# Optimization experiments

Hardware: AMD Instinct MI355X
Metric: run time of the kernel (lower is better)

The kernel has to match this reference:

```python
import jax, jax.numpy as jnp
import numpy as np

B, S, T, M, D, H = 32, 256, 400, 80, 512, 8


def setup_inputs() -> dict:
    ks = iter(jax.random.split(jax.random.key(0), 64))
    rn = lambda shape, s=0.05: jax.random.normal(next(ks), shape, jnp.float32) * s
    z = lambda shape: jnp.zeros(shape, jnp.float32)
    o = lambda shape: jnp.ones(shape, jnp.float32)
    inp = {
        'encoder_outputs': jax.random.normal(next(ks), (B, S, D), jnp.float32),
        'mel_targets': jax.random.normal(next(ks), (B, T, M), jnp.float32),
        'W_in': rn((M, D)), 'b_in': z(D),
        'Wq': rn((D, D)), 'bq': z(D),
        'Wk': rn((D, D)), 'bk': z(D),
        'Wv': rn((D, D)), 'bv': z(D),
        'Wo': rn((D, D)), 'bo': z(D),
        'W_ih0': rn((4 * D, D + M)), 'W_hh0': rn((4 * D, D)), 'b_ih0': z(4 * D), 'b_hh0': z(4 * D),
        'W_ih1': rn((4 * D, D)), 'W_hh1': rn((4 * D, D)), 'b_ih1': z(4 * D), 'b_hh1': z(4 * D),
        'W_mel': rn((D, M)), 'b_mel': z(M),
        'W_stop': rn((D, 1)), 'b_stop': z(1),
        'pw0': rn((512, M, 5)), 'pb0': z(512),
        'pw1': rn((512, 512, 5)), 'pb1': z(512),
        'pw2': rn((512, 512, 5)), 'pb2': z(512),
        'pw3': rn((512, 512, 5)), 'pb3': z(512),
        'pw4': rn((M, 512, 5)), 'pb4': z(M),
        'g0': o(512), 'be0': z(512), 'g1': o(512), 'be1': z(512),
        'g2': o(512), 'be2': z(512), 'g3': o(512), 'be3': z(512),
    }
    return inp


def _lstm_layer(x, W_ih, W_hh, b_ih, b_hh):
    # x: [B,T,I]. Precompute input contribution for all steps (big matmul), scan only recurrence.
    xg = jnp.einsum('bti,gi->btg', x, W_ih) + b_ih + b_hh  # [B,T,4D]
    Dh = W_hh.shape[1]

    def step(carry, xg_t):
        h, c = carry
        gates = xg_t + h @ W_hh.T
        i, f, g, o_ = jnp.split(gates, 4, axis=-1)  # pytorch gate order i,f,g,o
        c = jax.nn.sigmoid(f) * c + jax.nn.sigmoid(i) * jnp.tanh(g)
        h = jax.nn.sigmoid(o_) * jnp.tanh(c)
        return (h, c), h

    h0 = jnp.zeros((x.shape[0], Dh), x.dtype)
    _, hs = jax.lax.scan(step, (h0, h0), jnp.swapaxes(xg, 0, 1))
    return jnp.swapaxes(hs, 0, 1)  # [B,T,D]


def _conv1d(x, w, b):
    # x: [B,C,T], w: [O,I,K]
    y = jax.lax.conv_general_dilated(x, w, (1,), 'SAME', dimension_numbers=('NCH', 'OIH', 'NCH'))
    return y + b[None, :, None]


def _bn(x, g, be, eps=1e-5):
    # training-mode BatchNorm1d over (N, L) per channel
    mu = jnp.mean(x, axis=(0, 2), keepdims=True)
    var = jnp.mean((x - mu) ** 2, axis=(0, 2), keepdims=True)
    return (x - mu) * jax.lax.rsqrt(var + eps) * g[None, :, None] + be[None, :, None]


def _forward(encoder_outputs, mel_targets, W_in, b_in, Wq, bq, Wk, bk, Wv, bv, Wo, bo,
             W_ih0, W_hh0, b_ih0, b_hh0, W_ih1, W_hh1, b_ih1, b_hh1,
             W_mel, b_mel, W_stop, b_stop,
             pw0, pb0, pw1, pb1, pw2, pb2, pw3, pb3, pw4, pb4,
             g0, be0, g1, be1, g2, be2, g3, be3):
    Bs, Ts, Ms = mel_targets.shape
    Ss = encoder_outputs.shape[1]
    Ds = W_in.shape[1]
    Dh = Ds // H
    # teacher forcing: decoder input at step t is mel_targets[t-1], zeros at t=0
    dec_in = jnp.concatenate([jnp.zeros((Bs, 1, Ms), mel_targets.dtype), mel_targets[:, :-1]], axis=1)
    q_in = dec_in @ W_in + b_in  # [B,T,D]
    qh = (q_in @ Wq + bq).reshape(Bs, Ts, H, Dh)
    kh = (encoder_outputs @ Wk + bk).reshape(Bs, Ss, H, Dh)
    vh = (encoder_outputs @ Wv + bv).reshape(Bs, Ss, H, Dh)
    scores = jnp.einsum('bthd,bshd->bhts', qh, kh) / jnp.sqrt(jnp.float32(Dh))
    attn = jax.nn.softmax(scores, axis=-1)
    ctx = jnp.einsum('bhts,bshd->bthd', attn, vh).reshape(Bs, Ts, Ds)
    attn_out = ctx @ Wo + bo  # [B,T,D]
    lstm_in = jnp.concatenate([attn_out, dec_in], axis=-1)  # [B,T,D+M]
    h1 = _lstm_layer(lstm_in, W_ih0, W_hh0, b_ih0, b_hh0)
    h2 = _lstm_layer(h1, W_ih1, W_hh1, b_ih1, b_hh1)
    mel_outputs = h2 @ W_mel + b_mel   # [B,T,M]
    stop_outputs = h2 @ W_stop + b_stop  # [B,T,1]
    # postnet (dropout omitted; BN in training mode uses batch stats)
    x = jnp.swapaxes(mel_outputs, 1, 2)  # [B,M,T]
    x = jnp.tanh(_bn(_conv1d(x, pw0, pb0), g0, be0))
    x = jnp.tanh(_bn(_conv1d(x, pw1, pb1), g1, be1))
    x = jnp.tanh(_bn(_conv1d(x, pw2, pb2), g2, be2))
    x = jnp.tanh(_bn(_conv1d(x, pw3, pb3), g3, be3))
    x = _conv1d(x, pw4, pb4)
    mel_postnet = mel_outputs + jnp.swapaxes(x, 1, 2)
    return mel_outputs, mel_postnet, stop_outputs


def reference(encoder_outputs, mel_targets, W_in, b_in, Wq, bq, Wk, bk, Wv, bv, Wo, bo,
              W_ih0, W_hh0, b_ih0, b_hh0, W_ih1, W_hh1, b_ih1, b_hh1,
              W_mel, b_mel, W_stop, b_stop,
              pw0, pb0, pw1, pb1, pw2, pb2, pw3, pb3, pw4, pb4,
              g0, be0, g1, be1, g2, be2, g3, be3):
    return _forward(encoder_outputs, mel_targets, W_in, b_in, Wq, bq, Wk, bk, Wv, bv, Wo, bo,
                    W_ih0, W_hh0, b_ih0, b_hh0, W_ih1, W_hh1, b_ih1, b_hh1,
                    W_mel, b_mel, W_stop, b_stop,
                    pw0, pb0, pw1, pb1, pw2, pb2, pw3, pb3, pw4, pb4,
                    g0, be0, g1, be1, g2, be2, g3, be3)
```

## Files before the change

kernel.cpp:

```cpp
#include <hip/hip_runtime.h>
#include <math.h>

#define B_  32
#define S_  256
#define T_  400
#define M_  80
#define D_  512
#define H_  8
#define DH  64
#define BT  (B_*T_)
#define BS  (B_*S_)
#define G4  (4*D_)
#define DM  (D_+M_)
#define NB_ 96

typedef short s16x8 __attribute__((ext_vector_type(8)));
typedef float f32x4 __attribute__((ext_vector_type(4)));
typedef unsigned long long u64;

__device__ __forceinline__ unsigned short f2bf(float f) {
    union { float f; unsigned u; } v; v.f = f;
    unsigned r = v.u + 0x7fffu + ((v.u >> 16) & 1u);
    return (unsigned short)(r >> 16);
}
__device__ __forceinline__ float us2f(unsigned short u) {
    union { unsigned i; float f; } v; v.i = ((unsigned)u) << 16; return v.f;
}
__device__ __forceinline__ uint4 pack8(const float* f) {
    uint4 u;
    u.x = (unsigned)f2bf(f[0]) | ((unsigned)f2bf(f[1]) << 16);
    u.y = (unsigned)f2bf(f[2]) | ((unsigned)f2bf(f[3]) << 16);
    u.z = (unsigned)f2bf(f[4]) | ((unsigned)f2bf(f[5]) << 16);
    u.w = (unsigned)f2bf(f[6]) | ((unsigned)f2bf(f[7]) << 16);
    return u;
}
__device__ __forceinline__ u64 aload(const u64* p) {
    return __hip_atomic_load(p, __ATOMIC_RELAXED, __HIP_MEMORY_SCOPE_AGENT);
}
__device__ __forceinline__ void astore(u64* p, u64 v) {
    __hip_atomic_store(p, v, __ATOMIC_RELAXED, __HIP_MEMORY_SCOPE_AGENT);
}

__global__ __launch_bounds__(256) void k_prep(
    const float* __restrict__ bih1, const float* __restrict__ bhh1,
    float* __restrict__ bsum1,
    int* __restrict__ flags, int* __restrict__ hx2i,
    float* __restrict__ ssum, float* __restrict__ ssq)
{
    int i = blockIdx.x * 256 + threadIdx.x;
    if (i < G4) bsum1[i] = bih1[i] + bhh1[i];
    if (i < 512) { ssum[i] = 0.f; ssq[i] = 0.f; }
    if (i < NB_ * 32) flags[i] = 0;
    if (i < 2 * 32 * 512 / 2) hx2i[i] = 0;
}

__global__ __launch_bounds__(256) void k_w_c4(
    const float* s0, unsigned short* d0p, int n0,
    const float* s1, unsigned short* d1p, int n1,
    const float* s2, unsigned short* d2p, int n2,
    const float* s3, unsigned short* d3p, int n3)
{
    const float* s; unsigned short* d; int n;
    switch (blockIdx.y) {
        case 0: s = s0; d = d0p; n = n0; break;
        case 1: s = s1; d = d1p; n = n1; break;
        case 2: s = s2; d = d2p; n = n2; break;
        default: s = s3; d = d3p; n = n3; break;
    }
    int i = blockIdx.x * 256 + threadIdx.x;
    if (i < n) d[i] = f2bf(s[i]);
}
__global__ __launch_bounds__(256) void k_w_perm0(
    const float* __restrict__ W, unsigned short* __restrict__ dst,
    const float* __restrict__ bih, const float* __restrict__ bhh,
    float* __restrict__ bsum0p)
{
    int i = blockIdx.x * 256 + threadIdx.x;
    if (i < G4 * DM) {
        int np = i / DM, k = i - np * DM;
        int bd = np >> 6, r = np & 63, g = r >> 4, dl = r & 15;
        int ns = g * 512 + bd * 16 + dl;
        dst[i] = f2bf(W[(size_t)ns * DM + k]);
    }
    if (i < G4) {
        int bd = i >> 6, r = i & 63, g = r >> 4, dl = r & 15;
        int ns = g * 512 + bd * 16 + dl;
        bsum0p[i] = bih[ns] + bhh[ns];
    }
}
__global__ __launch_bounds__(256) void k_w_t4(
    const float* s0, unsigned short* d0p, int K0, int N0,
    const float* s1, unsigned short* d1p, int K1, int N1,
    const float* s2, unsigned short* d2p, int K2, int N2,
    const float* s3, unsigned short* d3p, int K3, int N3)
{
    const float* s; unsigned short* d; int K, N;
    switch (blockIdx.y) {
        case 0: s = s0; d = d0p; K = K0; N = N0; break;
        case 1: s = s1; d = d1p; K = K1; N = N1; break;
        case 2: s = s2; d = d2p; K = K2; N = N2; break;
        default: s = s3; d = d3p; K = K3; N = N3; break;
    }
    int i = blockIdx.x * 256 + threadIdx.x;
    if (i < K * N) {
        int n = i / K, k = i - n * K;
        d[i] = f2bf(s[(size_t)k * N + n]);
    }
}
__global__ __launch_bounds__(256) void k_w_conv5(
    const float* s0, unsigned short* d0p, int O0, int C0,
    const float* s1, unsigned short* d1p, int O1, int C1,
    const float* s2, unsigned short* d2p, int O2, int C2,
    const float* s3, unsigned short* d3p, int O3, int C3,
    const float* s4, unsigned short* d4p, int O4, int C4)
{
    const float* s; unsigned short* d; int O, C;
    switch (blockIdx.y) {
        case 0: s = s0; d = d0p; O = O0; C = C0; break;
        case 1: s = s1; d = d1p; O = O1; C = C1; break;
        case 2: s = s2; d = d2p; O = O2; C = C2; break;
        case 3: s = s3; d = d3p; O = O3; C = C3; break;
        default: s = s4; d = d4p; O = O4; C = C4; break;
    }
    int i = blockIdx.x * 256 + threadIdx.x;
    int n = O * C * 5;
    if (i < n) {
        int o = i / (5 * C), rem = i - o * 5 * C;
        int k = rem / C, c = rem - k * C;
        d[i] = f2bf(s[(size_t)o * C * 5 + c * 5 + k]);
    }
}

__global__ __launch_bounds__(256) void k_weff(
    const float* __restrict__ W_in, const float* __restrict__ Wq,
    const float* __restrict__ b_in, const float* __restrict__ bq,
    float* __restrict__ Weff, float* __restrict__ beff)
{
    int idx = blockIdx.x * 256 + threadIdx.x;
    if (idx < M_ * D_) {
        int m = idx / D_, d = idx - m * D_;
        float acc = 0.f;
        for (int j = 0; j < D_; ++j)
            acc += W_in[(size_t)m * D_ + j] * Wq[(size_t)j * D_ + d];
        Weff[idx] = acc;
    }
    if (idx < D_) {
        float acc = bq[idx];
        for (int j = 0; j < D_; ++j)
            acc += b_in[j] * Wq[(size_t)j * D_ + idx];
        beff[idx] = acc;
    }
}

__global__ __launch_bounds__(256) void k_mfma(
    const void* __restrict__ Aptr, int lda, const float* __restrict__ mel, int srcC,
    const unsigned short* __restrict__ Bt,
    void* __restrict__ Cptr, int ldc, const float* __restrict__ bias,
    int M, int N, int K, int mode, int abf16, int cbf16)
{
    __shared__ unsigned short As[128][40];
    __shared__ unsigned short Bs[128][40];
    int tid = threadIdx.x;
    int m0 = blockIdx.x * 128, n0 = blockIdx.y * 128;
    int wave = tid >> 6, lane = tid & 63;
    int wm = (wave >> 1) * 64, wn = (wave & 1) * 64;
    int l15 = lane & 15, quad = lane >> 4;

    f32x4 acc[4][4] = {};

    int srow = tid >> 1, half = tid & 1;
    int arow = m0 + srow;
    bool mok = arow < M;
    int arc = mok ? arow : 0;

    const float* Af = (const float*)Aptr;
    const unsigned short* Ab = (const unsigned short*)Aptr;
    const float* Arow_f = nullptr; const unsigned short* Arow_b = nullptr;
    const float* Mrow = nullptr;
    int bA = 0, tA = 0;
    if (mode == 2) { bA = arc / T_; tA = arc - bA * T_; }
    else {
        if (abf16) Arow_b = Ab + (size_t)arc * lda;
        else       Arow_f = Af + (size_t)arc * lda;
        if (mode == 1) {
            int tt = arc % T_;
            if (tt > 0) Mrow = mel + (size_t)(arc - 1) * M_;
        }
    }
    int brow = n0 + srow;
    bool nok = brow < N;
    const unsigned short* Brow = Bt + (size_t)(nok ? brow : 0) * K;
    const uint4 z4 = make_uint4(0, 0, 0, 0);

    for (int k0 = 0; k0 < K; k0 += 32) {
        int ks = k0 + half * 16;
        uint4 a0, a1;
        if (!mok || ks >= K) { a0 = z4; a1 = z4; }
        else if (mode == 2) {
            int sg = ks / srcC;
            int cc = ks - sg * srcC;
            int tt = tA + sg - 2;
            if (tt >= 0 && tt < T_) {
                float tf[16];
                const float4* s = (const float4*)(Af + (size_t)(bA * T_ + tt) * srcC + cc);
                #pragma unroll
                for (int i = 0; i < 4; ++i) {
                    float4 v = s[i];
                    tf[i*4+0] = v.x; tf[i*4+1] = v.y; tf[i*4+2] = v.z; tf[i*4+3] = v.w;
                }
                a0 = pack8(tf); a1 = pack8(tf + 8);
            } else { a0 = z4; a1 = z4; }
        } else if (abf16) {
            const uint4* s = (const uint4*)(Arow_b + ks);
            a0 = s[0]; a1 = s[1];
        } else if (mode == 1 && ks >= D_) {
            if (Mrow) {
                float tf[16];
                const float4* s = (const float4*)(Mrow + (ks - D_));
                #pragma unroll
                for (int i = 0; i < 4; ++i) {
                    float4 v = s[i];
                    tf[i*4+0] = v.x; tf[i*4+1] = v.y; tf[i*4+2] = v.z; tf[i*4+3] = v.w;
                }
                a0 = pack8(tf); a1 = pack8(tf + 8);
            } else { a0 = z4; a1 = z4; }
        } else {
            float tf[16];
            const float4* s = (const float4*)(Arow_f + ks);
            #pragma unroll
            for (int i = 0; i < 4; ++i) {
                float4 v = s[i];
                tf[i*4+0] = v.x; tf[i*4+1] = v.y; tf[i*4+2] = v.z; tf[i*4+3] = v.w;
            }
            a0 = pack8(tf); a1 = pack8(tf + 8);
        }
        *(uint4*)&As[srow][half * 16]     = a0;
        *(uint4*)&As[srow][half * 16 + 8] = a1;

        uint4 b0, b1;
        if (!nok || ks >= K) { b0 = z4; b1 = z4; }
        else {
            const uint4* s = (const uint4*)(Brow + ks);
            b0 = s[0]; b1 = s[1];
        }
        *(uint4*)&Bs[srow][half * 16]     = b0;
        *(uint4*)&Bs[srow][half * 16 + 8] = b1;
        __syncthreads();

        s16x8 af[4], bfr[4];
        #pragma unroll
        for (int i = 0; i < 4; ++i)
            af[i] = *(const s16x8*)&As[wm + i * 16 + l15][quad * 8];
        #pragma unroll
        for (int j = 0; j < 4; ++j)
            bfr[j] = *(const s16x8*)&Bs[wn + j * 16 + l15][quad * 8];
        #pragma unroll
        for (int i = 0; i < 4; ++i)
            #pragma unroll
            for (int j = 0; j < 4; ++j)
                acc[i][j] = __builtin_amdgcn_mfma_f32_16x16x32_bf16(af[i], bfr[j], acc[i][j], 0, 0, 0);
        __syncthreads();
    }

    #pragma unroll
    for (int i = 0; i < 4; ++i) {
        #pragma unroll
        for (int j = 0; j < 4; ++j) {
            int col = n0 + wn + j * 16 + l15;
            if (col >= N) continue;
            float bv = bias ? bias[col] : 0.f;
            #pragma unroll
            for (int r = 0; r < 4; ++r) {
                int row = m0 + wm + i * 16 + quad * 4 + r;
                if (row >= M) continue;
                float v = acc[i][j][r] + bv;
                if (cbf16) ((unsigned short*)Cptr)[(size_t)row * ldc + col] = f2bf(v);
                else       ((float*)Cptr)[(size_t)row * ldc + col] = v;
            }
        }
    }
}

__global__ __launch_bounds__(256) void k_attn(
    const float* __restrict__ mel,
    const float* __restrict__ Weff, const float* __restrict__ beff,
    const float* __restrict__ Kb, const float* __restrict__ Vb,
    float* __restrict__ ctx)
{
    __shared__ float mrow[4][80];
    __shared__ float qs[4][64];
    __shared__ float ps[4][256];
    int w = threadIdx.x >> 6, lane = threadIdx.x & 63;
    int row = blockIdx.x * 4 + w;
    int t = row % T_; int bh = row / T_;
    int h = bh % H_;  int b = bh / H_;

    {
        float v = 0.f;
        if (t > 0) v = mel[(size_t)(b * T_ + (t - 1)) * M_ + lane];
        mrow[w][lane] = v;
        if (lane < 16) {
            float v2 = 0.f;
            if (t > 0) v2 = mel[(size_t)(b * T_ + (t - 1)) * M_ + 64 + lane];
            mrow[w][64 + lane] = v2;
        }
    }
    __syncthreads();
    {
        int d = h * DH + lane;
        float q = beff[d];
        #pragma unroll 8
        for (int m = 0; m < M_; ++m) q += mrow[w][m] * Weff[(size_t)m * D_ + d];
        qs[w][lane] = q;
    }
    __syncthreads();

    const float* Kbase = Kb + (size_t)(b * S_) * D_ + h * DH;
    float sc[4];
    #pragma unroll
    for (int i = 0; i < 4; ++i) {
        int s = lane + i * 64;
        const float4* kr = (const float4*)(Kbase + (size_t)s * D_);
        float acc = 0.f;
        #pragma unroll
        for (int c4 = 0; c4 < 16; ++c4) {
            float4 kv = kr[c4];
            acc += qs[w][c4 * 4 + 0] * kv.x + qs[w][c4 * 4 + 1] * kv.y
                 + qs[w][c4 * 4 + 2] * kv.z + qs[w][c4 * 4 + 3] * kv.w;
        }
        sc[i] = acc * 0.125f;
    }
    float mx = fmaxf(fmaxf(sc[0], sc[1]), fmaxf(sc[2], sc[3]));
    #pragma unroll
    for (int off = 32; off; off >>= 1) mx = fmaxf(mx, __shfl_xor(mx, off, 64));
    float sum = 0.f;
    #pragma unroll
    for (int i = 0; i < 4; ++i) { sc[i] = __expf(sc[i] - mx); sum += sc[i]; }
    #pragma unroll
    for (int off = 32; off; off >>= 1) sum += __shfl_xor(sum, off, 64);
    float inv = 1.f / sum;
    #pragma unroll
    for (int i = 0; i < 4; ++i) ps[w][lane + i * 64] = sc[i] * inv;
    __syncthreads();

    const float* Vbase = Vb + (size_t)(b * S_) * D_ + h * DH + lane;
    float acc = 0.f;
    for (int s = 0; s < S_; ++s) acc += ps[w][s] * Vbase[(size_t)s * D_];
    ctx[(size_t)(b * T_ + t) * D_ + h * DH + lane] = acc;
}

__global__ __launch_bounds__(256) void k_lstm2(
    const unsigned short* __restrict__ xg0,
    const unsigned short* __restrict__ Whh0,
    const unsigned short* __restrict__ Wih1,
    const unsigned short* __restrict__ Whh1,
    const float* __restrict__ bsum1,
    unsigned short* __restrict__ hx1,
    unsigned short* __restrict__ hx2,
    unsigned short* __restrict__ h2seq,
    int* __restrict__ flags)
{
    __shared__ char smem[137856];
    int tid = threadIdx.x;
    int bid = blockIdx.x;
    int lane = tid & 63, wv = tid >> 6;
    int l15 = lane & 15, quad = lane >> 4;

    if (bid < 32) {
        unsigned short* Ws   = (unsigned short*)smem;
        unsigned short* hs   = Ws + 64 * 520;
        float*          gl   = (float*)(smem + 99840);
        unsigned short* hout = (unsigned short*)(smem + 108288);
        int d0 = bid * 16;
        {
            int r = tid >> 2, seg = tid & 3;
            int g = r >> 4, d = r & 15;
            const uint4* src = (const uint4*)(Whh0 + ((size_t)(g * 512 + d0 + d) * 512) + seg * 128);
            uint4* dst = (uint4*)(Ws + r * 520 + seg * 128);
            #pragma unroll
            for (int j = 0; j < 16; ++j) dst[j] = src[j];
        }
        int b_u = tid >> 3, dp = tid & 7;
        float c0r = 0.f, c1r = 0.f;
        __syncthreads();

        for (int i = 0; i <= 400; ++i) {
            if (i < 400) {
                int t = i;
                unsigned xv[4];
                {
                    const unsigned short* xr = xg0 + ((size_t)(b_u * T_ + t) * G4) + bid * 64;
                    #pragma unroll
                    for (int g = 0; g < 4; ++g) xv[g] = *(const unsigned*)(xr + g * 16 + 2 * dp);
                }
                if (t > 0) {
                    const u64* hrd = (const u64*)(hx1 + ((t + 1) & 1) * (32 * 512));
                    #pragma unroll
                    for (int it = 0; it < 8; ++it) {
                        int u = it * 256 + tid;
                        int row = u >> 6, c8 = u & 63;
                        u64 lo = aload(hrd + 2 * u);
                        u64 hi = aload(hrd + 2 * u + 1);
                        u64* d = (u64*)(hs + row * 520 + c8 * 8);
                        d[0] = lo; d[1] = hi;
                    }
                    __syncthreads();
                    f32x4 acc0 = {}, acc1 = {};
                    #pragma unroll
                    for (int k0 = 0; k0 < 512; k0 += 32) {
                        s16x8 af = *(const s16x8*)(Ws + (wv * 16 + l15) * 520 + k0 + quad * 8);
                        s16x8 b0 = *(const s16x8*)(hs + l15 * 520 + k0 + quad * 8);
                        s16x8 b1 = *(const s16x8*)(hs + (16 + l15) * 520 + k0 + quad * 8);
                        acc0 = __builtin_amdgcn_mfma_f32_16x16x32_bf16(af, b0, acc0, 0, 0, 0);
                        acc1 = __builtin_amdgcn_mfma_f32_16x16x32_bf16(af, b1, acc1, 0, 0, 0);
                    }
                    #pragma unroll
                    for (int r = 0; r < 4; ++r) {
                        gl[(wv * 16 + quad * 4 + r) * 33 + l15]      = acc0[r];
                        gl[(wv * 16 + quad * 4 + r) * 33 + 16 + l15] = acc1[r];
                    }
                }
                __syncthreads();
                {
                    float h2v[2];
                    #pragma unroll
                    for (int q = 0; q < 2; ++q) {
                        int d = 2 * dp + q;
                        float iv = us2f((unsigned short)(xv[0] >> (16 * q)));
                        float fv = us2f((unsigned short)(xv[1] >> (16 * q)));
                        float gv = us2f((unsigned short)(xv[2] >> (16 * q)));
                        float ov = us2f((unsigned short)(xv[3] >> (16 * q)));
                        if (t > 0) {
                            iv += gl[(0 * 16 + d) * 33 + b_u];
                            fv += gl[(1 * 16 + d) * 33 + b_u];
                            gv += gl[(2 * 16 + d) * 33 + b_u];
                            ov += gl[(3 * 16 + d) * 33 + b_u];
                        }
                        float si = 1.f / (1.f + __expf(-iv));
                        float sf = 1.f / (1.f + __expf(-fv));
                        float so = 1.f / (1.f + __expf(-ov));
                        float tg = tanhf(gv);
                        float cold = (t > 0) ? (q ? c1r : c0r) : 0.f;
                        float c = sf * cold + si * tg;
                        float h = so * tanhf(c);
                        if (q) c1r = c; else c0r = c;
                        h2v[q] = h;
                    }
                    unsigned pk = (unsigned)f2bf(h2v[0]) | ((unsigned)f2bf(h2v[1]) << 16);
                    *(unsigned*)(hout + b_u * 16 + 2 * dp) = pk;
                }
                __syncthreads();
                if (tid < 64) {
                    int b = tid >> 1, hf = tid & 1;
                    uint4 v = *(const uint4*)(hout + b * 16 + hf * 8);
                    u64 lo = ((u64)v.y << 32) | v.x;
                    u64 hi = ((u64)v.w << 32) | v.z;
                    u64* dst = (u64*)(hx1 + (t & 1) * (32 * 512) + (size_t)b * 512 + d0 + hf * 8);
                    astore(dst, lo); astore(dst + 1, hi);
                }
            }
            if (i < 400) {
                __syncthreads();
                if (tid == 0)
                    __hip_atomic_store(flags + bid * 32, i + 1, __ATOMIC_RELAXED, __HIP_MEMORY_SCOPE_AGENT);
                if (tid < NB_) {
                    while (__hip_atomic_load(flags + tid * 32, __ATOMIC_RELAXED, __HIP_MEMORY_SCOPE_AGENT) < i + 1)
                        __builtin_amdgcn_s_sleep(1);
                }
                __syncthreads();
            }
        }
    } else {
        unsigned short* Wc    = (unsigned short*)smem;
        unsigned short* hcat  = Wc + 32 * 1040;
        float*          gl1   = (float*)(smem + 133120);
        unsigned short* hout1 = (unsigned short*)(smem + 137344);
        int bd1 = bid - 32;
        int d0 = bd1 * 8;
        {
            int r = tid >> 3, seg = tid & 7;
            int g = r >> 3, d = r & 7;
            const unsigned short* wsrc = ((seg < 4) ? Wih1 : Whh1)
                + (size_t)(g * 512 + d0 + d) * 512 + (seg & 3) * 128;
            uint4* wdst = (uint4*)(Wc + r * 1040 + seg * 128);
            const uint4* ws4 = (const uint4*)wsrc;
            #pragma unroll
            for (int j = 0; j < 16; ++j) wdst[j] = ws4[j];
        }
        int dd = tid >> 5, b_u = tid & 31;
        float bs[4];
        #pragma unroll
        for (int g = 0; g < 4; ++g) bs[g] = bsum1[g * 512 + d0 + dd];
        int mt = wv >> 1, nt = wv & 1;
        float creg = 0.f;
        __syncthreads();

        for (int i = 0; i <= 400; ++i) {
            if (i >= 1) {
                int t = i - 1;
                const u64* s1 = (const u64*)(hx1 + ((i - 1) & 1) * (32 * 512));
                const u64* s2 = (const u64*)(hx2 + ((i - 2) & 1) * (32 * 512));
                #pragma unroll
                for (int it = 0; it < 8; ++it) {
                    int u = it * 256 + tid;
                    int row = u >> 6, c8 = u & 63;
                    u64 lo = aload(s1 + 2 * u), hi = aload(s1 + 2 * u + 1);
                    u64* d = (u64*)(hcat + row * 1040 + c8 * 8);
                    d[0] = lo; d[1] = hi;
                    lo = aload(s2 + 2 * u); hi = aload(s2 + 2 * u + 1);
                    d = (u64*)(hcat + row * 1040 + 512 + c8 * 8);
                    d[0] = lo; d[1] = hi;
                }
                __syncthreads();
                f32x4 acc = {};
                #pragma unroll 4
                for (int k0 = 0; k0 < 1024; k0 += 32) {
                    s16x8 af = *(const s16x8*)(Wc + (mt * 16 + l15) * 1040 + k0 + quad * 8);
                    s16x8 bf = *(const s16x8*)(hcat + (nt * 16 + l15) * 1040 + k0 + quad * 8);
                    acc = __builtin_amdgcn_mfma_f32_16x16x32_bf16(af, bf, acc, 0, 0, 0);
                }
                #pragma unroll
                for (int r = 0; r < 4; ++r)
                    gl1[(mt * 16 + quad * 4 + r) * 33 + nt * 16 + l15] = acc[r];
                __syncthreads();
                {
                    float iv = gl1[(0 * 8 + dd) * 33 + b_u] + bs[0];
                    float fv = gl1[(1 * 8 + dd) * 33 + b_u] + bs[1];
                    float gv = gl1[(2 * 8 + dd) * 33 + b_u] + bs[2];
                    float ov = gl1[(3 * 8 + dd) * 33 + b_u] + bs[3];
                    float si = 1.f / (1.f + __expf(-iv));
                    float sf = 1.f / (1.f + __expf(-fv));
                    float so = 1.f / (1.f + __expf(-ov));
                    float tg = tanhf(gv);
                    float cold = (t > 0) ? creg : 0.f;
                    float c = sf * cold + si * tg;
                    float h = so * tanhf(c);
                    creg = c;
                    hout1[b_u * 8 + dd] = f2bf(h);
                }
                __syncthreads();
                if (tid < 32) {
                    uint4 v = *(const uint4*)(hout1 + tid * 8);
                    u64 lo = ((u64)v.y << 32) | v.x;
                    u64 hi = ((u64)v.w << 32) | v.z;
                    u64* dst = (u64*)(hx2 + (t & 1) * (32 * 512) + (size_t)tid * 512 + d0);
                    astore(dst, lo); astore(dst + 1, hi);
                    *(uint4*)(h2seq + ((size_t)tid * T_ + t) * 512 + d0) = v;
                }
            }
            if (i < 400) {
                __syncthreads();
                if (tid == 0)
                    __hip_atomic_store(flags + bid * 32, i + 1, __ATOMIC_RELAXED, __HIP_MEMORY_SCOPE_AGENT);
                if (tid < NB_) {
                    while (__hip_atomic_load(flags + tid * 32, __ATOMIC_RELAXED, __HIP_MEMORY_SCOPE_AGENT) < i + 1)
                        __builtin_amdgcn_s_sleep(1);
                }
                __syncthreads();
            }
        }
    }
}

__global__ __launch_bounds__(256) void k_stop(
    const unsigned short* __restrict__ h2, const float* __restrict__ W,
    const float* __restrict__ bsc, float* __restrict__ out)
{
    int w = threadIdx.x >> 6, lane = threadIdx.x & 63;
    int row = blockIdx.x * 4 + w;
    const unsigned short* hr = h2 + (size_t)row * 512 + lane * 8;
    float acc = 0.f;
    #pragma unroll
    for (int j = 0; j < 8; ++j) acc += us2f(hr[j]) * W[lane * 8 + j];
    #pragma unroll
    for (int off = 32; off; off >>= 1) acc += __shfl_xor(acc, off, 64);
    if (lane == 0) out[row] = acc + bsc[0];
}

__global__ __launch_bounds__(256) void k_stats_part(
    const float* __restrict__ x, float* __restrict__ ssum, float* __restrict__ ssq)
{
    int r0 = blockIdx.x * 50;
    int c1 = threadIdx.x, c2 = threadIdx.x + 256;
    float s1 = 0.f, q1 = 0.f, s2 = 0.f, q2 = 0.f;
    for (int r = r0; r < r0 + 50; ++r) {
        float v1 = x[(size_t)r * 512 + c1]; s1 += v1; q1 += v1 * v1;
        float v2 = x[(size_t)r * 512 + c2]; s2 += v2; q2 += v2 * v2;
    }
    atomicAdd(&ssum[c1], s1); atomicAdd(&ssq[c1], q1);
    atomicAdd(&ssum[c2], s2); atomicAdd(&ssq[c2], q2);
}
__global__ __launch_bounds__(256) void k_stats_fin(
    float* __restrict__ ssum, float* __restrict__ ssq,
    const float* __restrict__ gw, const float* __restrict__ bw,
    float* __restrict__ scale, float* __restrict__ shift)
{
    int c = blockIdx.x * 256 + threadIdx.x;
    if (c < 512) {
        float mean = ssum[c] / (float)BT;
        float var  = ssq[c] / (float)BT - mean * mean;
        float scv  = gw[c] * rsqrtf(var + 1e-5f);
        scale[c] = scv;
        shift[c] = bw[c] - mean * scv;
        ssum[c] = 0.f; ssq[c] = 0.f;
    }
}

__global__ __launch_bounds__(256) void k_bnact(
    float* __restrict__ x, int C,
    const float* __restrict__ scale, const float* __restrict__ shift)
{
    int idx = blockIdx.x * 256 + threadIdx.x;
    if (idx < BT * C) {
        int c = idx % C;
        x[idx] = tanhf(scale[c] * x[idx] + shift[c]);
    }
}

__global__ __launch_bounds__(256) void k_residual(
    const float* __restrict__ mel, float* __restrict__ out)
{
    int i = blockIdx.x * 256 + threadIdx.x;
    if (i < BT * M_) out[i] += mel[i];
}

extern "C" void kernel_launch(void* const* d_in, const int* in_sizes, int n_in,
                              void* d_out, int out_size, void* d_ws, size_t ws_size,
                              hipStream_t stream)
{
    const float* enc    = (const float*)d_in[0];
    const float* mel_t  = (const float*)d_in[1];
    const float* W_in   = (const float*)d_in[2];
    const float* b_in   = (const float*)d_in[3];
    const float* Wq     = (const float*)d_in[4];  const float* bq = (const float*)d_in[5];
    const float* Wk     = (const float*)d_in[6];  const float* bk = (const float*)d_in[7];
    const float* Wv     = (const float*)d_in[8];  const float* bv = (const float*)d_in[9];
    const float* Wo     = (const float*)d_in[10]; const float* bo = (const float*)d_in[11];
    const float* W_ih0  = (const float*)d_in[12]; const float* W_hh0 = (const float*)d_in[13];
    const float* b_ih0  = (const float*)d_in[14]; const float* b_hh0 = (const float*)d_in[15];
    const float* W_ih1  = (const float*)d_in[16]; const float* W_hh1 = (const float*)d_in[17];
    const float* b_ih1  = (const float*)d_in[18]; const float* b_hh1 = (const float*)d_in[19];
    const float* W_mel  = (const float*)d_in[20]; const float* b_mel = (const float*)d_in[21];
    const float* W_stop = (const float*)d_in[22]; const float* b_stop = (const float*)d_in[23];
    const float* pw0 = (const float*)d_in[24]; const float* pb0 = (const float*)d_in[25];
    const float* pw1 = (const float*)d_in[26]; const float* pb1 = (const float*)d_in[27];
    const float* pw2 = (const float*)d_in[28]; const float* pb2 = (const float*)d_in[29];
    const float* pw3 = (const float*)d_in[30]; const float* pb3 = (const float*)d_in[31];
    const float* pw4 = (const float*)d_in[32]; const float* pb4 = (const float*)d_in[33];
    const float* g0 = (const float*)d_in[34]; const float* be0 = (const float*)d_in[35];
    const float* g1 = (const float*)d_in[36]; const float* be1 = (const float*)d_in[37];
    const float* g2 = (const float*)d_in[38]; const float* be2 = (const float*)d_in[39];
    const float* g3 = (const float*)d_in[40]; const float* be3 = (const float*)d_in[41];

    char* p = (char*)d_ws;
    float* Kb  = (float*)(p + 0);
    float* Vb  = (float*)(p + 16777216);
    float* ctx = (float*)(p + 33554432);
    float* ao  = (float*)(p + 0);
    unsigned short* xg0   = (unsigned short*)(p + 26214400);
    unsigned short* h2seq = (unsigned short*)(p + 0);
    float* p_a = (float*)(p + 13107200);
    float* p_b = (float*)(p + 39321600);
    size_t off = 78643200;
    float* bsum0 = (float*)(p + off); off += 8192;
    float* bsum1 = (float*)(p + off); off += 8192;
    unsigned short* hx1 = (unsigned short*)(p + off); off += 65536;
    unsigned short* hx2 = (unsigned short*)(p + off); off += 65536;
    int* flags = (int*)(p + off); off += 12288;
    float* beff = (float*)(p + off); off += 2048;
    float* Weff = (float*)(p + off); off += 163840;
    float* sc0 = (float*)(p + off); off += 2048;
    float* sh0 = (float*)(p + off); off += 2048;
    float* sc1 = (float*)(p + off); off += 2048;
    float* sh1 = (float*)(p + off); off += 2048;
    float* sc2 = (float*)(p + off); off += 2048;
    float* sh2 = (float*)(p + off); off += 2048;
    float* sc3 = (float*)(p + off); off += 2048;
    float* sh3 = (float*)(p + off); off += 2048;
    float* ssum = (float*)(p + off); off += 2048;
    float* ssq  = (float*)(p + off); off += 2048;
    unsigned short* Wk_t   = (unsigned short*)(p + off); off += 524288;
    unsigned short* Wv_t   = (unsigned short*)(p + off); off += 524288;
    unsigned short* Wo_t   = (unsigned short*)(p + off); off += 524288;
    unsigned short* Wmel_t = (unsigned short*)(p + off); off += 81920;
    unsigned short* Wih0_b = (unsigned short*)(p + off); off += 2424832;
    unsigned short* Wih1_b = (unsigned short*)(p + off); off += 2097152;
    unsigned short* Whh0_b = (unsigned short*)(p + off); off += 2097152;
    unsigned short* Whh1_b = (unsigned short*)(p + off); off += 2097152;
    unsigned short* pw0_b  = (unsigned short*)(p + off); off += 409600;
    unsigned short* pw1_b  = (unsigned short*)(p + off); off += 2621440;
    unsigned short* pw2_b  = (unsigned short*)(p + off); off += 2621440;
    unsigned short* pw3_b  = (unsigned short*)(p + off); off += 2621440;
    unsigned short* pw4_b  = (unsigned short*)(p + off); off += 409600;

    float* out_mel  = (float*)d_out;
    float* out_post = out_mel + (size_t)BT * M_;
    float* out_stop = out_post + (size_t)BT * M_;

    dim3 blk(256);
    auto MF = [&](const void* A, int lda, const float* mel, int srcC,
                  const unsigned short* Bt, void* C, int ldc, const float* bias,
                  int M, int N, int K, int mode, int abf16, int cbf16) {
        dim3 g((M + 127) / 128, (N + 127) / 128);
        k_mfma<<<g, blk, 0, stream>>>(A, lda, mel, srcC, Bt, C, ldc, bias, M, N, K, mode, abf16, cbf16);
    };

    k_prep<<<128, blk, 0, stream>>>(b_ih1, b_hh1, bsum1, flags, (int*)hx2, ssum, ssq);
    k_weff<<<160, blk, 0, stream>>>(W_in, Wq, b_in, bq, Weff, beff);
    k_w_perm0<<<4736, blk, 0, stream>>>(W_ih0, Wih0_b, b_ih0, b_hh0, bsum0);
    {
        dim3 gc(4096, 4);
        k_w_c4<<<gc, blk, 0, stream>>>(W_ih1, Wih1_b, G4 * D_,
                                       W_hh0, Whh0_b, G4 * D_,
                                       W_hh1, Whh1_b, G4 * D_,
                                       W_ih1, Wih1_b, G4 * D_);
        dim3 gt(1024, 4);
        k_w_t4<<<gt, blk, 0, stream>>>(Wk, Wk_t, D_, D_,
                                       Wv, Wv_t, D_, D_,
                                       Wo, Wo_t, D_, D_,
                                       W_mel, Wmel_t, D_, M_);
        dim3 gv(5120, 5);
        k_w_conv5<<<gv, blk, 0, stream>>>(pw0, pw0_b, 512, 80,
                                          pw1, pw1_b, 512, 512,
                                          pw2, pw2_b, 512, 512,
                                          pw3, pw3_b, 512, 512,
                                          pw4, pw4_b, 80, 512);
    }

    MF(enc, D_, nullptr, 0, Wk_t, Kb, D_, bk, BS, D_, D_, 0, 0, 0);
    MF(enc, D_, nullptr, 0, Wv_t, Vb, D_, bv, BS, D_, D_, 0, 0, 0);

    k_attn<<<(B_ * H_ * T_) / 4, blk, 0, stream>>>(mel_t, Weff, beff, Kb, Vb, ctx);

    MF(ctx, D_, nullptr, 0, Wo_t, ao, D_, bo, BT, D_, D_, 0, 0, 0);

    MF(ao, D_, mel_t, 0, Wih0_b, xg0, G4, bsum0, BT, G4, DM, 1, 0, 1);

    k_lstm2<<<NB_, blk, 0, stream>>>(xg0, Whh0_b, Wih1_b, Whh1_b, bsum1,
                                     hx1, hx2, h2seq, flags);

    MF(h2seq, D_, nullptr, 0, Wmel_t, out_mel, M_, b_mel, BT, M_, D_, 0, 1, 0);
    k_stop<<<BT / 4, blk, 0, stream>>>(h2seq, W_stop, b_stop, out_stop);

    int gD = (BT * D_ + 255) / 256;

    MF(out_mel, 0, nullptr, M_, pw0_b, p_a, D_, pb0, BT, D_, M_ * 5, 2, 0, 0);
    k_stats_part<<<256, blk, 0, stream>>>(p_a, ssum, ssq);
    k_stats_fin<<<2, blk, 0, stream>>>(ssum, ssq, g0, be0, sc0, sh0);
    k_bnact<<<gD, blk, 0, stream>>>(p_a, D_, sc0, sh0);

    MF(p_a, 0, nullptr, D_, pw1_b, p_b, D_, pb1, BT, D_, D_ * 5, 2, 0, 0);
    k_stats_part<<<256, blk, 0, stream>>>(p_b, ssum, ssq);
    k_stats_fin<<<2, blk, 0, stream>>>(ssum, ssq, g1, be1, sc1, sh1);
    k_bnact<<<gD, blk, 0, stream>>>(p_b, D_, sc1, sh1);

    MF(p_b, 0, nullptr, D_, pw2_b, p_a, D_, pb2, BT, D_, D_ * 5, 2, 0, 0);
    k_stats_part<<<256, blk, 0, stream>>>(p_a, ssum, ssq);
    k_stats_fin<<<2, blk, 0, stream>>>(ssum, ssq, g2, be2, sc2, sh2);
    k_bnact<<<gD, blk, 0, stream>>>(p_a, D_, sc2, sh2);

    MF(p_a, 0, nullptr, D_, pw3_b, p_b, D_, pb3, BT, D_, D_ * 5, 2, 0, 0);
    k_stats_part<<<256, blk, 0, stream>>>(p_b, ssum, ssq);
    k_stats_fin<<<2, blk, 0, stream>>>(ssum, ssq, g3, be3, sc3, sh3);
    k_bnact<<<gD, blk, 0, stream>>>(p_b, D_, sc3, sh3);

    MF(p_b, 0, nullptr, D_, pw4_b, out_post, M_, pb4, BT, M_, D_ * 5, 2, 0, 0);
    k_residual<<<4000, blk, 0, stream>>>(out_mel, out_post);
}
```

Before: 4.294 ms.

## Fuse BN stats and residual into GEMM epilogue, store attention K/V/ctx as bf16

The postnet GEMM epilogue now accumulates per-column sum and sum-of-squares into shared memory, then atomically into the global stats buffers. This removes the separate stats pass that re-read each 12800x512 activation. The final conv adds the mel residual in its epilogue, which drops the residual kernel. K, V and the attention context are now stored in bf16 to halve their traffic in the attention and Wo GEMM, at some cost in precision.

```diff
diff --git a/kernel.cpp b/kernel.cpp
--- a/kernel.cpp
+++ b/kernel.cpp
@@ -34,6 +34,12 @@
     u.w = (unsigned)f2bf(f[6]) | ((unsigned)f2bf(f[7]) << 16);
     return u;
 }
+__device__ __forceinline__ void bf8_dec(const uint4 u, float* f) {
+    f[0] = us2f(u.x & 0xffffu); f[1] = us2f(u.x >> 16);
+    f[2] = us2f(u.y & 0xffffu); f[3] = us2f(u.y >> 16);
+    f[4] = us2f(u.z & 0xffffu); f[5] = us2f(u.z >> 16);
+    f[6] = us2f(u.w & 0xffffu); f[7] = us2f(u.w >> 16);
+}
 __device__ __forceinline__ u64 aload(const u64* p) {
     return __hip_atomic_load(p, __ATOMIC_RELAXED, __HIP_MEMORY_SCOPE_AGENT);
 }
@@ -156,15 +162,21 @@
     const void* __restrict__ Aptr, int lda, const float* __restrict__ mel, int srcC,
     const unsigned short* __restrict__ Bt,
     void* __restrict__ Cptr, int ldc, const float* __restrict__ bias,
-    int M, int N, int K, int mode, int abf16, int cbf16)
+    int M, int N, int K, int mode, int abf16, int cbf16,
+    float* __restrict__ ssum_o, float* __restrict__ ssq_o,
+    const float* __restrict__ resid)
 {
     __shared__ unsigned short As[128][40];
     __shared__ unsigned short Bs[128][40];
+    __shared__ float colsum[128];
+    __shared__ float colsq[128];
     int tid = threadIdx.x;
     int m0 = blockIdx.x * 128, n0 = blockIdx.y * 128;
     int wave = tid >> 6, lane = tid & 63;
     int wm = (wave >> 1) * 64, wn = (wave & 1) * 64;
     int l15 = lane & 15, quad = lane >> 4;
+
+    if (ssum_o && tid < 128) { colsum[tid] = 0.f; colsq[tid] = 0.f; }
 
     f32x4 acc[4][4] = {};
 
@@ -269,14 +281,35 @@
             int col = n0 + wn + j * 16 + l15;
             if (col >= N) continue;
             float bv = bias ? bias[col] : 0.f;
+            float s_acc = 0.f, q_acc = 0.f;
             #pragma unroll
             for (int r = 0; r < 4; ++r) {
                 int row = m0 + wm + i * 16 + quad * 4 + r;
                 if (row >= M) continue;
                 float v = acc[i][j][r] + bv;
+                if (resid) v += resid[(size_t)row * ldc + col];
+                s_acc += v; q_acc += v * v;
                 if (cbf16) ((unsigned short*)Cptr)[(size_t)row * ldc + col] = f2bf(v);
                 else       ((float*)Cptr)[(size_t)row * ldc + col] = v;
             }
+            if (ssum_o) {
+                s_acc += __shfl_xor(s_acc, 16, 64); s_acc += __shfl_xor(s_acc, 32, 64);
+                q_acc += __shfl_xor(q_acc, 16, 64); q_acc += __shfl_xor(q_acc, 32, 64);
+                if (quad == 0) {
+                    atomicAdd(&colsum[wn + j * 16 + l15], s_acc);
+                    atomicAdd(&colsq [wn + j * 16 + l15], q_acc);
+                }
+            }
+        }
+    }
+    if (ssum_o) {
+        __syncthreads();
+        if (tid < 128) {
+            int col = n0 + tid;
+            if (col < N) {
+                atomicAdd(&ssum_o[col], colsum[tid]);
+                atomicAdd(&ssq_o[col],  colsq[tid]);
+            }
         }
     }
 }
@@ -284,8 +317,8 @@
 __global__ __launch_bounds__(256) void k_attn(
     const float* __restrict__ mel,
     const float* __restrict__ Weff, const float* __restrict__ beff,
-    const float* __restrict__ Kb, const float* __restrict__ Vb,
-    float* __restrict__ ctx)
+    const unsigned short* __restrict__ Kb, const unsigned short* __restrict__ Vb,
+    unsigned short* __restrict__ ctx)
 {
     __shared__ float mrow[4][80];
     __shared__ float qs[4][64];
@@ -315,18 +348,19 @@
     }
     __syncthreads();
 
-    const float* Kbase = Kb + (size_t)(b * S_) * D_ + h * DH;
+    const unsigned short* Kbase = Kb + (size_t)(b * S_) * D_ + h * DH;
     float sc[4];
     #pragma unroll
     for (int i = 0; i < 4; ++i) {
         int s = lane + i * 64;
-        const float4* kr = (const float4*)(Kbase + (size_t)s * D_);
+        const uint4* kr = (const uint4*)(Kbase + (size_t)s * D_);
         float acc = 0.f;
         #pragma unroll
-        for (int c4 = 0; c4 < 16; ++c4) {
-            float4 kv = kr[c4];
-            acc += qs[w][c4 * 4 + 0] * kv.x + qs[w][c4 * 4 + 1] * kv.y
-                 + qs[w][c4 * 4 + 2] * kv.z + qs[w][c4 * 4 + 3] * kv.w;
+        for (int c8 = 0; c8 < 8; ++c8) {
+            uint4 u = kr[c8];
+            float kv[8]; bf8_dec(u, kv);
+            #pragma unroll
+            for (int j = 0; j < 8; ++j) acc += qs[w][c8 * 8 + j] * kv[j];
         }
         sc[i] = acc * 0.125f;
     }
@@ -343,10 +377,10 @@
     for (int i = 0; i < 4; ++i) ps[w][lane + i * 64] = sc[i] * inv;
     __syncthreads();
 
-    const float* Vbase = Vb + (size_t)(b * S_) * D_ + h * DH + lane;
+    const unsigned short* Vbase = Vb + (size_t)(b * S_) * D_ + h * DH + lane;
     float acc = 0.f;
-    for (int s = 0; s < S_; ++s) acc += ps[w][s] * Vbase[(size_t)s * D_];
-    ctx[(size_t)(b * T_ + t) * D_ + h * DH + lane] = acc;
+    for (int s = 0; s < S_; ++s) acc += ps[w][s] * us2f(Vbase[(size_t)s * D_]);
+    ctx[(size_t)(b * T_ + t) * D_ + h * DH + lane] = f2bf(acc);
 }
 
 __global__ __launch_bounds__(256) void k_lstm2(
@@ -577,19 +611,6 @@
     if (lane == 0) out[row] = acc + bsc[0];
 }
 
-__global__ __launch_bounds__(256) void k_stats_part(
-    const float* __restrict__ x, float* __restrict__ ssum, float* __restrict__ ssq)
-{
-    int r0 = blockIdx.x * 50;
-    int c1 = threadIdx.x, c2 = threadIdx.x + 256;
-    float s1 = 0.f, q1 = 0.f, s2 = 0.f, q2 = 0.f;
-    for (int r = r0; r < r0 + 50; ++r) {
-        float v1 = x[(size_t)r * 512 + c1]; s1 += v1; q1 += v1 * v1;
-        float v2 = x[(size_t)r * 512 + c2]; s2 += v2; q2 += v2 * v2;
-    }
-    atomicAdd(&ssum[c1], s1); atomicAdd(&ssq[c1], q1);
-    atomicAdd(&ssum[c2], s2); atomicAdd(&ssq[c2], q2);
-}
 __global__ __launch_bounds__(256) void k_stats_fin(
     float* __restrict__ ssum, float* __restrict__ ssq,
     const float* __restrict__ gw, const float* __restrict__ bw,
@@ -615,13 +636,6 @@
         int c = idx % C;
         x[idx] = tanhf(scale[c] * x[idx] + shift[c]);
     }
-}
-
-__global__ __launch_bounds__(256) void k_residual(
-    const float* __restrict__ mel, float* __restrict__ out)
-{
-    int i = blockIdx.x * 256 + threadIdx.x;
-    if (i < BT * M_) out[i] += mel[i];
 }
 
 extern "C" void kernel_launch(void* const* d_in, const int* in_sizes, int n_in,
@@ -653,9 +667,9 @@
     const float* g3 = (const float*)d_in[40]; const float* be3 = (const float*)d_in[41];
 
     char* p = (char*)d_ws;
-    float* Kb  = (float*)(p + 0);
-    float* Vb  = (float*)(p + 16777216);
-    float* ctx = (float*)(p + 33554432);
+    unsigned short* Kb  = (unsigned short*)(p + 0);
+    unsigned short* Vb  = (unsigned short*)(p + 16777216);
+    unsigned short* ctx = (unsigned short*)(p + 33554432);
     float* ao  = (float*)(p + 0);
     unsigned short* xg0   = (unsigned short*)(p + 26214400);
     unsigned short* h2seq = (unsigned short*)(p + 0);
@@ -700,9 +714,11 @@
     dim3 blk(256);
     auto MF = [&](const void* A, int lda, const float* mel, int srcC,
                   const unsigned short* Bt, void* C, int ldc, const float* bias,
-                  int M, int N, int K, int mode, int abf16, int cbf16) {
+                  int M, int N, int K, int mode, int abf16, int cbf16,
+                  float* so, float* sq, const float* rs) {
         dim3 g((M + 127) / 128, (N + 127) / 128);
-        k_mfma<<<g, blk, 0, stream>>>(A, lda, mel, srcC, Bt, C, ldc, bias, M, N, K, mode, abf16, cbf16);
+        k_mfma<<<g, blk, 0, stream>>>(A, lda, mel, srcC, Bt, C, ldc, bias, M, N, K,
+                                      mode, abf16, cbf16, so, sq, rs);
     };
 
     k_prep<<<128, blk, 0, stream>>>(b_ih1, b_hh1, bsum1, flags, (int*)hx2, ssum, ssq);
@@ -727,43 +743,38 @@
                                           pw4, pw4_b, 80, 512);
     }
 
-    MF(enc, D_, nullptr, 0, Wk_t, Kb, D_, bk, BS, D_, D_, 0, 0, 0);
-    MF(enc, D_, nullptr, 0, Wv_t, Vb, D_, bv, BS, D_, D_, 0, 0, 0);
+    MF(enc, D_, nullptr, 0, Wk_t, Kb, D_, bk, BS, D_, D_, 0, 0, 1, nullptr, nullptr, nullptr);
+    MF(enc, D_, nullptr, 0, Wv_t, Vb, D_, bv, BS, D_, D_, 0, 0, 1, nullptr, nullptr, nullptr);
 
     k_attn<<<(B_ * H_ * T_) / 4, blk, 0, stream>>>(mel_t, Weff, beff, Kb, Vb, ctx);
 
-    MF(ctx, D_, nullptr, 0, Wo_t, ao, D_, bo, BT, D_, D_, 0, 0, 0);
-
-    MF(ao, D_, mel_t, 0, Wih0_b, xg0, G4, bsum0, BT, G4, DM, 1, 0, 1);
+    MF(ctx, D_, nullptr, 0, Wo_t, ao, D_, bo, BT, D_, D_, 0, 1, 0, nullptr, nullptr, nullptr);
+
+    MF(ao, D_, mel_t, 0, Wih0_b, xg0, G4, bsum0, BT, G4, DM, 1, 0, 1, nullptr, nullptr, nullptr);
 
     k_lstm2<<<NB_, blk, 0, stream>>>(xg0, Whh0_b, Wih1_b, Whh1_b, bsum1,
                                      hx1, hx2, h2seq, flags);
 
-    MF(h2seq, D_, nullptr, 0, Wmel_t, out_mel, M_, b_mel, BT, M_, D_, 0, 1, 0);
+    MF(h2seq, D_, nullptr, 0, Wmel_t, out_mel, M_, b_mel, BT, M_, D_, 0, 1, 0, nullptr, nullptr, nullptr);
     k_stop<<<BT / 4, blk, 0, stream>>>(h2seq, W_stop, b_stop, out_stop);
 
     int gD = (BT * D_ + 255) / 256;
 
-    MF(out_mel, 0, nullptr, M_, pw0_b, p_a, D_, pb0, BT, D_, M_ * 5, 2, 0, 0);
-    k_stats_part<<<256, blk, 0, stream>>>(p_a, ssum, ssq);
+    MF(out_mel, 0, nullptr, M_, pw0_b, p_a, D_, pb0, BT, D_, M_ * 5, 2, 0, 0, ssum, ssq, nullptr);
     k_stats_fin<<<2, blk, 0, stream>>>(ssum, ssq, g0, be0, sc0, sh0);
     k_bnact<<<gD, blk, 0, stream>>>(p_a, D_, sc0, sh0);
 
-    MF(p_a, 0, nullptr, D_, pw1_b, p_b, D_, pb1, BT, D_, D_ * 5, 2, 0, 0);
-    k_stats_part<<<256, blk, 0, stream>>>(p_b, ssum, ssq);
+    MF(p_a, 0, nullptr, D_, pw1_b, p_b, D_, pb1, BT, D_, D_ * 5, 2, 0, 0, ssum, ssq, nullptr);
     k_stats_fin<<<2, blk, 0, stream>>>(ssum, ssq, g1, be1, sc1, sh1);
     k_bnact<<<gD, blk, 0, stream>>>(p_b, D_, sc1, sh1);
 
-    MF(p_b, 0, nullptr, D_, pw2_b, p_a, D_, pb2, BT, D_, D_ * 5, 2, 0, 0);
-    k_stats_part<<<256, blk, 0, stream>>>(p_a, ssum, ssq);
+    MF(p_b, 0, nullptr, D_, pw2_b, p_a, D_, pb2, BT, D_, D_ * 5, 2, 0, 0, ssum, ssq, nullptr);
     k_stats_fin<<<2, blk, 0, stream>>>(ssum, ssq, g2, be2, sc2, sh2);
     k_bnact<<<gD, blk, 0, stream>>>(p_a, D_, sc2, sh2);
 
-    MF(p_a, 0, nullptr, D_, pw3_b, p_b, D_, pb3, BT, D_, D_ * 5, 2, 0, 0);
-    k_stats_part<<<256, blk, 0, stream>>>(p_b, ssum, ssq);
+    MF(p_a, 0, nullptr, D_, pw3_b, p_b, D_, pb3, BT, D_, D_ * 5, 2, 0, 0, ssum, ssq, nullptr);
     k_stats_fin<<<2, blk, 0, stream>>>(ssum, ssq, g3, be3, sc3, sh3);
     k_bnact<<<gD, blk, 0, stream>>>(p_b, D_, sc3, sh3);
 
-    MF(p_b, 0, nullptr, D_, pw4_b, out_post, M_, pb4, BT, M_, D_ * 5, 2, 0, 0);
-    k_residual<<<4000, blk, 0, stream>>>(out_mel, out_post);
-}
+    MF(p_b, 0, nullptr, D_, pw4_b, out_post, M_, pb4, BT, M_, D_ * 5, 2, 0, 0, nullptr, nullptr, out_mel);
+}
```

Measured after the change: 3.843 ms. -10.5%, faster.
